# Kernel tuning notes

Hardware: AMD Instinct MI355X
Metric: run time of the kernel (lower is better)

Reference implementation:

```python
import jax, jax.numpy as jnp
import numpy as np

H = 1024   # context_size == review_len (code requires equality)
B = 64     # batch_size
T = 1024   # review_len


def setup_inputs() -> dict:
    key = jax.random.key(0)
    k1, k2 = jax.random.split(key)
    decoder_hidden = jax.random.normal(k1, (B, H), dtype=jnp.float32)
    # original indexes encoder_outputs[:, batch, t] -> vector of size H
    encoder_outputs = jax.random.normal(k2, (H, B, T), dtype=jnp.float32)
    return {"decoder_hidden": decoder_hidden, "encoder_outputs": encoder_outputs}


def reference(decoder_hidden, encoder_outputs):
    # score[b,t] = dot(decoder_hidden[b], encoder_outputs[:, b, t])  ('dot' method)
    scores = jnp.einsum('hbt,bh->bt', encoder_outputs, decoder_hidden)  # [B,T]
    # weighted[h,b,t] = encoder_outputs[h,b,t] * score[b,t]
    weighted = encoder_outputs * scores[None, :, :]                      # [H,B,T]
    # per t: softmax over hidden dim of the [B,H] matrix, then sum over t
    sm = jax.nn.softmax(weighted, axis=0)                                # softmax over H
    attn_energies = jnp.sum(sm, axis=2).T                                # [B,H] (== [B, review_len])
    return attn_energies
```

## Files before the change

kernel.cpp:

```cpp
#include <hip/hip_runtime.h>
#include <math.h>

#define H  1024
#define B  64
#define T  1024
#define BT (B*T)
#define TC 16
#define SPLIT 8
#define CHUNKS 8

__device__ __forceinline__ float ex2(float x) { return __builtin_amdgcn_exp2f(x); }

__global__ __launch_bounds__(256, 2) void attn_main(const float* __restrict__ dec,
                                                    const float* __restrict__ enc,
                                                    float* __restrict__ ws)
{
    __shared__ float tile[H * TC];
    __shared__ __align__(16) float rbuf[3][4][TC];
    __shared__ __align__(16) float prm[2][TC];

    const int tid   = threadIdx.x;
    const int split = blockIdx.x;
    const int b     = blockIdx.y;
    const int lane  = tid & 63;
    const int wave  = tid >> 6;

    const int r   = tid >> 2;
    const int c4  = tid & 3;
    const int cb1 = (5 * (r >> 1)) & 15;
    const int col0 = (4*c4 + 0 + cb1) & 15;
    const int col1 = (4*c4 + 1 + cb1) & 15;
    const int col2 = (4*c4 + 2 + cb1) & 15;
    const int col3 = (4*c4 + 3 + cb1) & 15;

    const int t2  = tid & 15;
    const int g   = tid >> 4;
    const int cb2 = (t2 + 5 * (g >> 1)) & 15;

    const int cb3 = (5 * (tid >> 1)) & 15;

    float acc0 = 0.f, acc1 = 0.f, acc2 = 0.f, acc3 = 0.f;

    const float L2E = 1.44269504088896340736f;

    for (int c = 0; c < CHUNKS; ++c) {
        const int t0 = (split * CHUNKS + c) * TC;
        __syncthreads();

        float4 s4  = make_float4(0.f, 0.f, 0.f, 0.f);
        float4 mx4 = make_float4(-INFINITY, -INFINITY, -INFINITY, -INFINITY);
        float4 mn4 = make_float4( INFINITY,  INFINITY,  INFINITY,  INFINITY);
        #pragma unroll
        for (int i = 0; i < 16; ++i) {
            const int h = r + 64*i;
            const float4 v = *(reinterpret_cast<const float4*>(enc + (size_t)h*BT + b*T + t0) + c4);
            const float dh = dec[b*H + h];
            s4.x = fmaf(v.x, dh, s4.x); s4.y = fmaf(v.y, dh, s4.y);
            s4.z = fmaf(v.z, dh, s4.z); s4.w = fmaf(v.w, dh, s4.w);
            mx4.x = fmaxf(mx4.x, v.x); mx4.y = fmaxf(mx4.y, v.y);
            mx4.z = fmaxf(mx4.z, v.z); mx4.w = fmaxf(mx4.w, v.w);
            mn4.x = fminf(mn4.x, v.x); mn4.y = fminf(mn4.y, v.y);
            mn4.z = fminf(mn4.z, v.z); mn4.w = fminf(mn4.w, v.w);
            const int base = h * TC;
            tile[base + col0] = v.x;
            tile[base + col1] = v.y;
            tile[base + col2] = v.z;
            tile[base + col3] = v.w;
        }
        #pragma unroll
        for (int off = 4; off <= 32; off <<= 1) {
            s4.x += __shfl_xor(s4.x, off); s4.y += __shfl_xor(s4.y, off);
            s4.z += __shfl_xor(s4.z, off); s4.w += __shfl_xor(s4.w, off);
            mx4.x = fmaxf(mx4.x, __shfl_xor(mx4.x, off)); mx4.y = fmaxf(mx4.y, __shfl_xor(mx4.y, off));
            mx4.z = fmaxf(mx4.z, __shfl_xor(mx4.z, off)); mx4.w = fmaxf(mx4.w, __shfl_xor(mx4.w, off));
            mn4.x = fminf(mn4.x, __shfl_xor(mn4.x, off)); mn4.y = fminf(mn4.y, __shfl_xor(mn4.y, off));
            mn4.z = fminf(mn4.z, __shfl_xor(mn4.z, off)); mn4.w = fminf(mn4.w, __shfl_xor(mn4.w, off));
        }
        if (lane < 4) {
            *reinterpret_cast<float4*>(&rbuf[0][wave][lane*4]) = s4;
            *reinterpret_cast<float4*>(&rbuf[1][wave][lane*4]) = mx4;
            *reinterpret_cast<float4*>(&rbuf[2][wave][lane*4]) = mn4;
        }
        __syncthreads();
        if (tid < TC) {
            const float s  = rbuf[0][0][tid] + rbuf[0][1][tid] + rbuf[0][2][tid] + rbuf[0][3][tid];
            const float mx = fmaxf(fmaxf(rbuf[1][0][tid], rbuf[1][1][tid]),
                                   fmaxf(rbuf[1][2][tid], rbuf[1][3][tid]));
            const float mn = fminf(fminf(rbuf[2][0][tid], rbuf[2][1][tid]),
                                   fminf(rbuf[2][2][tid], rbuf[2][3][tid]));
            const float m  = (s >= 0.f) ? s*mx : s*mn;
            prm[0][tid] = s * L2E;
            prm[1][tid] = m * L2E;
        }
        __syncthreads();

        {
            const float s2 = prm[0][t2];
            const float m2 = prm[1][t2];
            const int b0 = g*TC + cb2;
            const int b1 = g*TC + (cb2 ^ 8);
            float dp = 0.f;
            #pragma unroll
            for (int i = 0; i < 64; ++i) {
                const int idx = ((i & 1) ? b1 : b0) + 256*i;
                const float e  = tile[idx];
                const float ev = ex2(fmaf(e, s2, -m2));
                dp += ev;
                tile[idx] = ev;
            }
            dp += __shfl_xor(dp, 16);
            dp += __shfl_xor(dp, 32);
            if (lane < TC) rbuf[0][wave][lane] = dp;
        }
        __syncthreads();
        if (tid < TC) {
            const float d = rbuf[0][0][tid] + rbuf[0][1][tid] + rbuf[0][2][tid] + rbuf[0][3][tid];
            prm[0][tid] = 1.0f / d;
        }
        __syncthreads();

        {
            const float4 r0 = *reinterpret_cast<const float4*>(&prm[0][0]);
            const float4 r1 = *reinterpret_cast<const float4*>(&prm[0][4]);
            const float4 r2 = *reinterpret_cast<const float4*>(&prm[0][8]);
            const float4 r3 = *reinterpret_cast<const float4*>(&prm[0][12]);
            const float rp[16] = { r0.x,r0.y,r0.z,r0.w, r1.x,r1.y,r1.z,r1.w,
                                   r2.x,r2.y,r2.z,r2.w, r3.x,r3.y,r3.z,r3.w };
            #pragma unroll
            for (int k = 0; k < 4; ++k) {
                const int h    = tid + 256*k;
                const int base = h * TC;
                float a = 0.f;
                int q = cb3;
                #pragma unroll
                for (int p = 0; p < 16; ++p) {
                    a = fmaf(tile[base + q], rp[p], a);
                    q = (q + 1) & 15;
                }
                if (k == 0) acc0 += a; else if (k == 1) acc1 += a;
                else if (k == 2) acc2 += a; else acc3 += a;
            }
        }
    }

    const size_t wbase = (size_t)(b * SPLIT + split) * H;
    ws[wbase + tid      ] = acc0;
    ws[wbase + tid + 256] = acc1;
    ws[wbase + tid + 512] = acc2;
    ws[wbase + tid + 768] = acc3;
}

__global__ __launch_bounds__(256) void attn_reduce(const float* __restrict__ ws,
                                                   float* __restrict__ out)
{
    const int idx = blockIdx.x * 256 + threadIdx.x;
    const int b = idx >> 10;
    const int h = idx & 1023;
    float s = 0.f;
    #pragma unroll
    for (int sp = 0; sp < SPLIT; ++sp)
        s += ws[(size_t)(b * SPLIT + sp) * H + h];
    out[idx] = s;
}

extern "C" void kernel_launch(void* const* d_in, const int* in_sizes, int n_in,
                              void* d_out, int out_size, void* d_ws, size_t ws_size,
                              hipStream_t stream)
{
    const float* dec = (const float*)d_in[0];
    const float* enc = (const float*)d_in[1];
    float* out = (float*)d_out;
    float* ws  = (float*)d_ws;

    attn_main  <<<dim3(SPLIT, B), 256, 0, stream>>>(dec, enc, ws);
    attn_reduce<<<dim3((B*H)/256), 256, 0, stream>>>(ws, out);
}
```

Measured before the change: 391.6 us.

## Keep encoder chunk in registers instead of LDS tile, widen chunk to 32

Removes the large shared-memory tile. Each thread now keeps its 16 float4 encoder values in registers across the score, exp and weighted-sum phases, and the final per-h sums are reduced with lane shuffles. The block grows to 512 threads and each chunk spans 32 timesteps, so every row read is 128 contiguous bytes instead of 64. This is meant to cut LDS traffic and the occupancy limit the 64KB tile imposed, at the cost of higher register pressure and an extra cross-lane reduction at the end.

```diff
diff --git a/kernel.cpp b/kernel.cpp
--- a/kernel.cpp
+++ b/kernel.cpp
@@ -5,70 +5,55 @@
 #define B  64
 #define T  1024
 #define BT (B*T)
-#define TC 16
+#define TC 32
 #define SPLIT 8
-#define CHUNKS 8
+#define CHUNKS 4
+#define NT 512
 
 __device__ __forceinline__ float ex2(float x) { return __builtin_amdgcn_exp2f(x); }
 
-__global__ __launch_bounds__(256, 2) void attn_main(const float* __restrict__ dec,
-                                                    const float* __restrict__ enc,
-                                                    float* __restrict__ ws)
+__global__ __launch_bounds__(NT, 4) void attn_main(const float* __restrict__ dec,
+                                                   const float* __restrict__ enc,
+                                                   float* __restrict__ ws)
 {
-    __shared__ float tile[H * TC];
-    __shared__ __align__(16) float rbuf[3][4][TC];
-    __shared__ __align__(16) float prm[2][TC];
+    __shared__ float rbuf[3][8][TC];
+    __shared__ float prm[2][TC];
 
     const int tid   = threadIdx.x;
     const int split = blockIdx.x;
     const int b     = blockIdx.y;
     const int lane  = tid & 63;
     const int wave  = tid >> 6;
-
-    const int r   = tid >> 2;
-    const int c4  = tid & 3;
-    const int cb1 = (5 * (r >> 1)) & 15;
-    const int col0 = (4*c4 + 0 + cb1) & 15;
-    const int col1 = (4*c4 + 1 + cb1) & 15;
-    const int col2 = (4*c4 + 2 + cb1) & 15;
-    const int col3 = (4*c4 + 3 + cb1) & 15;
-
-    const int t2  = tid & 15;
-    const int g   = tid >> 4;
-    const int cb2 = (t2 + 5 * (g >> 1)) & 15;
-
-    const int cb3 = (5 * (tid >> 1)) & 15;
-
-    float acc0 = 0.f, acc1 = 0.f, acc2 = 0.f, acc3 = 0.f;
+    const int r     = tid >> 3;
+    const int c8    = tid & 7;
 
     const float L2E = 1.44269504088896340736f;
 
+    float acc[16];
+    #pragma unroll
+    for (int i = 0; i < 16; ++i) acc[i] = 0.f;
+
     for (int c = 0; c < CHUNKS; ++c) {
         const int t0 = (split * CHUNKS + c) * TC;
-        __syncthreads();
 
+        float4 v[16];
         float4 s4  = make_float4(0.f, 0.f, 0.f, 0.f);
         float4 mx4 = make_float4(-INFINITY, -INFINITY, -INFINITY, -INFINITY);
         float4 mn4 = make_float4( INFINITY,  INFINITY,  INFINITY,  INFINITY);
         #pragma unroll
         for (int i = 0; i < 16; ++i) {
             const int h = r + 64*i;
-            const float4 v = *(reinterpret_cast<const float4*>(enc + (size_t)h*BT + b*T + t0) + c4);
+            v[i] = *reinterpret_cast<const float4*>(enc + (size_t)h*BT + b*T + t0 + 4*c8);
             const float dh = dec[b*H + h];
-            s4.x = fmaf(v.x, dh, s4.x); s4.y = fmaf(v.y, dh, s4.y);
-            s4.z = fmaf(v.z, dh, s4.z); s4.w = fmaf(v.w, dh, s4.w);
-            mx4.x = fmaxf(mx4.x, v.x); mx4.y = fmaxf(mx4.y, v.y);
-            mx4.z = fmaxf(mx4.z, v.z); mx4.w = fmaxf(mx4.w, v.w);
-            mn4.x = fminf(mn4.x, v.x); mn4.y = fminf(mn4.y, v.y);
-            mn4.z = fminf(mn4.z, v.z); mn4.w = fminf(mn4.w, v.w);
-            const int base = h * TC;
-            tile[base + col0] = v.x;
-            tile[base + col1] = v.y;
-            tile[base + col2] = v.z;
-            tile[base + col3] = v.w;
+            s4.x = fmaf(v[i].x, dh, s4.x); s4.y = fmaf(v[i].y, dh, s4.y);
+            s4.z = fmaf(v[i].z, dh, s4.z); s4.w = fmaf(v[i].w, dh, s4.w);
+            mx4.x = fmaxf(mx4.x, v[i].x); mx4.y = fmaxf(mx4.y, v[i].y);
+            mx4.z = fmaxf(mx4.z, v[i].z); mx4.w = fmaxf(mx4.w, v[i].w);
+            mn4.x = fminf(mn4.x, v[i].x); mn4.y = fminf(mn4.y, v[i].y);
+            mn4.z = fminf(mn4.z, v[i].z); mn4.w = fminf(mn4.w, v[i].w);
         }
         #pragma unroll
-        for (int off = 4; off <= 32; off <<= 1) {
+        for (int off = 8; off <= 32; off <<= 1) {
             s4.x += __shfl_xor(s4.x, off); s4.y += __shfl_xor(s4.y, off);
             s4.z += __shfl_xor(s4.z, off); s4.w += __shfl_xor(s4.w, off);
             mx4.x = fmaxf(mx4.x, __shfl_xor(mx4.x, off)); mx4.y = fmaxf(mx4.y, __shfl_xor(mx4.y, off));
@@ -76,78 +61,82 @@
             mn4.x = fminf(mn4.x, __shfl_xor(mn4.x, off)); mn4.y = fminf(mn4.y, __shfl_xor(mn4.y, off));
             mn4.z = fminf(mn4.z, __shfl_xor(mn4.z, off)); mn4.w = fminf(mn4.w, __shfl_xor(mn4.w, off));
         }
-        if (lane < 4) {
+        if (lane < 8) {
             *reinterpret_cast<float4*>(&rbuf[0][wave][lane*4]) = s4;
             *reinterpret_cast<float4*>(&rbuf[1][wave][lane*4]) = mx4;
             *reinterpret_cast<float4*>(&rbuf[2][wave][lane*4]) = mn4;
         }
         __syncthreads();
         if (tid < TC) {
-            const float s  = rbuf[0][0][tid] + rbuf[0][1][tid] + rbuf[0][2][tid] + rbuf[0][3][tid];
-            const float mx = fmaxf(fmaxf(rbuf[1][0][tid], rbuf[1][1][tid]),
-                                   fmaxf(rbuf[1][2][tid], rbuf[1][3][tid]));
-            const float mn = fminf(fminf(rbuf[2][0][tid], rbuf[2][1][tid]),
-                                   fminf(rbuf[2][2][tid], rbuf[2][3][tid]));
-            const float m  = (s >= 0.f) ? s*mx : s*mn;
+            float s  = rbuf[0][0][tid];
+            float mx = rbuf[1][0][tid];
+            float mn = rbuf[2][0][tid];
+            #pragma unroll
+            for (int w = 1; w < 8; ++w) {
+                s += rbuf[0][w][tid];
+                mx = fmaxf(mx, rbuf[1][w][tid]);
+                mn = fminf(mn, rbuf[2][w][tid]);
+            }
+            const float m = (s >= 0.f) ? s*mx : s*mn;
             prm[0][tid] = s * L2E;
             prm[1][tid] = m * L2E;
         }
         __syncthreads();
 
         {
-            const float s2 = prm[0][t2];
-            const float m2 = prm[1][t2];
-            const int b0 = g*TC + cb2;
-            const int b1 = g*TC + (cb2 ^ 8);
-            float dp = 0.f;
+            const float4 sv = *reinterpret_cast<const float4*>(&prm[0][c8*4]);
+            const float4 mv = *reinterpret_cast<const float4*>(&prm[1][c8*4]);
+            float4 d4 = make_float4(0.f, 0.f, 0.f, 0.f);
             #pragma unroll
-            for (int i = 0; i < 64; ++i) {
-                const int idx = ((i & 1) ? b1 : b0) + 256*i;
-                const float e  = tile[idx];
-                const float ev = ex2(fmaf(e, s2, -m2));
-                dp += ev;
-                tile[idx] = ev;
+            for (int i = 0; i < 16; ++i) {
+                v[i].x = ex2(fmaf(v[i].x, sv.x, -mv.x));
+                v[i].y = ex2(fmaf(v[i].y, sv.y, -mv.y));
+                v[i].z = ex2(fmaf(v[i].z, sv.z, -mv.z));
+                v[i].w = ex2(fmaf(v[i].w, sv.w, -mv.w));
+                d4.x += v[i].x; d4.y += v[i].y; d4.z += v[i].z; d4.w += v[i].w;
             }
-            dp += __shfl_xor(dp, 16);
-            dp += __shfl_xor(dp, 32);
-            if (lane < TC) rbuf[0][wave][lane] = dp;
+            #pragma unroll
+            for (int off = 8; off <= 32; off <<= 1) {
+                d4.x += __shfl_xor(d4.x, off); d4.y += __shfl_xor(d4.y, off);
+                d4.z += __shfl_xor(d4.z, off); d4.w += __shfl_xor(d4.w, off);
+            }
+            if (lane < 8)
+                *reinterpret_cast<float4*>(&rbuf[0][wave][lane*4]) = d4;
         }
         __syncthreads();
         if (tid < TC) {
-            const float d = rbuf[0][0][tid] + rbuf[0][1][tid] + rbuf[0][2][tid] + rbuf[0][3][tid];
+            float d = rbuf[0][0][tid];
+            #pragma unroll
+            for (int w = 1; w < 8; ++w) d += rbuf[0][w][tid];
             prm[0][tid] = 1.0f / d;
         }
         __syncthreads();
 
         {
-            const float4 r0 = *reinterpret_cast<const float4*>(&prm[0][0]);
-            const float4 r1 = *reinterpret_cast<const float4*>(&prm[0][4]);
-            const float4 r2 = *reinterpret_cast<const float4*>(&prm[0][8]);
-            const float4 r3 = *reinterpret_cast<const float4*>(&prm[0][12]);
-            const float rp[16] = { r0.x,r0.y,r0.z,r0.w, r1.x,r1.y,r1.z,r1.w,
-                                   r2.x,r2.y,r2.z,r2.w, r3.x,r3.y,r3.z,r3.w };
+            const float4 rv = *reinterpret_cast<const float4*>(&prm[0][c8*4]);
             #pragma unroll
-            for (int k = 0; k < 4; ++k) {
-                const int h    = tid + 256*k;
-                const int base = h * TC;
-                float a = 0.f;
-                int q = cb3;
-                #pragma unroll
-                for (int p = 0; p < 16; ++p) {
-                    a = fmaf(tile[base + q], rp[p], a);
-                    q = (q + 1) & 15;
-                }
-                if (k == 0) acc0 += a; else if (k == 1) acc1 += a;
-                else if (k == 2) acc2 += a; else acc3 += a;
+            for (int i = 0; i < 16; ++i) {
+                acc[i] = fmaf(v[i].x, rv.x, acc[i]);
+                acc[i] = fmaf(v[i].y, rv.y, acc[i]);
+                acc[i] = fmaf(v[i].z, rv.z, acc[i]);
+                acc[i] = fmaf(v[i].w, rv.w, acc[i]);
             }
         }
+        __syncthreads();
     }
 
+    #pragma unroll
+    for (int i = 0; i < 16; ++i) {
+        acc[i] += __shfl_xor(acc[i], 1);
+        acc[i] += __shfl_xor(acc[i], 2);
+        acc[i] += __shfl_xor(acc[i], 4);
+    }
     const size_t wbase = (size_t)(b * SPLIT + split) * H;
-    ws[wbase + tid      ] = acc0;
-    ws[wbase + tid + 256] = acc1;
-    ws[wbase + tid + 512] = acc2;
-    ws[wbase + tid + 768] = acc3;
+    #pragma unroll
+    for (int i = 0; i < 16; ++i) {
+        if ((i >> 1) == c8)
+            ws[wbase + r + 64*i] = acc[i];
+    }
 }
 
 __global__ __launch_bounds__(256) void attn_reduce(const float* __restrict__ ws,
@@ -172,6 +161,6 @@
     float* out = (float*)d_out;
     float* ws  = (float*)d_ws;
 
-    attn_main  <<<dim3(SPLIT, B), 256, 0, stream>>>(dec, enc, ws);
+    attn_main  <<<dim3(SPLIT, B), NT, 0, stream>>>(dec, enc, ws);
     attn_reduce<<<dim3((B*H)/256), 256, 0, stream>>>(ws, out);
 }
```

New measurement: 377.7 us. 1.04x faster.
